# Kernel optimization log

Hardware: AMD Instinct MI355X
Metric: run time of the kernel (lower is better)

The kernel has to match this reference:

```python
import jax, jax.numpy as jnp
import numpy as np

N = 8192      # nodes (= hidden_channels / heads)
E = 262144    # edges (avg degree 32)
IN = 256      # in_channels
H = 8         # heads
C = 32        # out_channels per head
NEG_SLOPE = 0.2


def setup_inputs() -> dict:
    key = jax.random.key(0)
    ks = jax.random.split(key, 8)
    x = jax.random.normal(ks[0], (N, IN), jnp.float32)
    edge_index = jax.random.randint(ks[1], (2, E), 0, N, dtype=jnp.int32)
    lin_w = jax.random.normal(ks[2], (H * C, IN), jnp.float32) * (1.0 / np.sqrt(IN))
    att_src = jax.random.normal(ks[3], (H, C), jnp.float32) * 0.1
    att_dst = jax.random.normal(ks[4], (H, C), jnp.float32) * 0.1
    bias = jax.random.normal(ks[5], (H * C,), jnp.float32) * 0.01
    out_w = jax.random.normal(ks[6], (C, N * H * C), jnp.float32) * (1.0 / np.sqrt(N * H * C))
    out_b = jax.random.normal(ks[7], (C,), jnp.float32) * 0.01
    return {"x": x, "edge_index": edge_index, "lin_w": lin_w, "att_src": att_src,
            "att_dst": att_dst, "bias": bias, "out_w": out_w, "out_b": out_b}


def reference(x, edge_index, lin_w, att_src, att_dst, bias, out_w, out_b):
    n = x.shape[0]
    # PyG GATConv default: add self loops
    loop = jnp.arange(n, dtype=edge_index.dtype)
    src = jnp.concatenate([edge_index[0], loop])  # message sources j
    dst = jnp.concatenate([edge_index[1], loop])  # message targets i
    # per-head linear projection: [n, H, C]
    xh = (x @ lin_w.T).reshape(n, H, C)
    a_src = jnp.einsum('nhc,hc->nh', xh, att_src)  # [n, H]
    a_dst = jnp.einsum('nhc,hc->nh', xh, att_dst)  # [n, H]
    # edge attention logits + segment softmax over incoming edges of each dst
    e = jax.nn.leaky_relu(a_src[src] + a_dst[dst], negative_slope=NEG_SLOPE)  # [E', H]
    m = jax.ops.segment_max(e, dst, num_segments=n)        # [n, H]
    ex = jnp.exp(e - m[dst])
    denom = jax.ops.segment_sum(ex, dst, num_segments=n)   # [n, H]
    alpha = ex / denom[dst]                                 # [E', H]
    # weighted scatter-add aggregation
    agg = jax.ops.segment_sum(alpha[:, :, None] * xh[src], dst, num_segments=n)  # [n, H, C]
    out = agg.reshape(n, H * C) + bias
    # flatten all nodes, dense output layer, softmax
    y = out.reshape(-1) @ out_w.T + out_b  # [C]
    return jax.nn.softmax(y)
```

## Files before the change

### kernel.cpp

```cpp
#include <hip/hip_runtime.h>


namespace {
constexpr int  kN    = 8192;
constexpr int  kE    = 262144;
constexpr int  kTotE = kE + kN;
constexpr long kK    = 2097152;
constexpr int  kNBF  = 2048;
}

typedef float vfloat4 __attribute__((ext_vector_type(4)));

static __device__ __forceinline__ ushort f2bf(float f) {
  unsigned u = __float_as_uint(f);
  return (ushort)((u + 0x7FFFu + ((u >> 16) & 1u)) >> 16);
}
static __device__ __forceinline__ float bf2f(ushort b) {
  return __uint_as_float(((unsigned)b) << 16);
}

__global__ __launch_bounds__(256) void gemm_xh(const float* __restrict__ x,
                                               const float* __restrict__ lw,
                                               float* __restrict__ xh,
                                               ushort* __restrict__ xh_bf) {
  __shared__ float As[16][68];
  __shared__ float Bs[16][68];
  const int t  = threadIdx.x;
  const int tx = t & 15, ty = t >> 4;
  const int rowBase = blockIdx.x * 64;
  const int colBase = blockIdx.y * 64;
  const int lr = t >> 2;
  const int lk = (t & 3) * 4;

  float acc[4][4] = {};
  for (int kc = 0; kc < 256; kc += 16) {
    float4 av = *(const float4*)(x  + (long)(rowBase + lr) * 256 + kc + lk);
    float4 bv = *(const float4*)(lw + (long)(colBase + lr) * 256 + kc + lk);
    __syncthreads();
    As[lk + 0][lr] = av.x; As[lk + 1][lr] = av.y; As[lk + 2][lr] = av.z; As[lk + 3][lr] = av.w;
    Bs[lk + 0][lr] = bv.x; Bs[lk + 1][lr] = bv.y; Bs[lk + 2][lr] = bv.z; Bs[lk + 3][lr] = bv.w;
    __syncthreads();
#pragma unroll
    for (int k = 0; k < 16; k++) {
      float4 a4 = *(const float4*)(&As[k][ty * 4]);
      float4 b4 = *(const float4*)(&Bs[k][tx * 4]);
      float aa[4] = {a4.x, a4.y, a4.z, a4.w};
      float bb[4] = {b4.x, b4.y, b4.z, b4.w};
#pragma unroll
      for (int i = 0; i < 4; i++)
#pragma unroll
        for (int j = 0; j < 4; j++) acc[i][j] += aa[i] * bb[j];
    }
  }
#pragma unroll
  for (int i = 0; i < 4; i++) {
    const long row = rowBase + ty * 4 + i;
    float4 o = make_float4(acc[i][0], acc[i][1], acc[i][2], acc[i][3]);
    *(float4*)(xh + row * 256 + colBase + tx * 4) = o;
    ushort4 ob = make_ushort4(f2bf(o.x), f2bf(o.y), f2bf(o.z), f2bf(o.w));
    *(ushort4*)(xh_bf + row * 256 + colBase + tx * 4) = ob;
  }
}

__global__ __launch_bounds__(256) void att_deg(const float* __restrict__ xh,
                                               const float* __restrict__ att_s,
                                               const float* __restrict__ att_d,
                                               const int* __restrict__ ei,
                                               float* __restrict__ a_src,
                                               float* __restrict__ a_dst,
                                               int* __restrict__ cnt) {
  const int n = blockIdx.x, t = threadIdx.x;
  float v = xh[(long)n * 256 + t];
  float s = v * att_s[t];
  float d = v * att_d[t];
#pragma unroll
  for (int off = 16; off; off >>= 1) {
    s += __shfl_down(s, off, 32);
    d += __shfl_down(d, off, 32);
  }
  if ((t & 31) == 0) {
    a_src[n * 8 + (t >> 5)] = s;
    a_dst[n * 8 + (t >> 5)] = d;
  }
  const int gid = n * 256 + t;
  if (gid < kE) atomicAdd(&cnt[ei[kE + gid]], 1);
}

__global__ __launch_bounds__(1024) void scan_cnt(const int* __restrict__ cnt,
                                                 int* __restrict__ rowptr,
                                                 int* __restrict__ wpos) {
  __shared__ int s[1024];
  const int t = threadIdx.x;
  int v[8]; int sum = 0;
#pragma unroll
  for (int q = 0; q < 8; q++) { v[q] = cnt[t * 8 + q] + 1; sum += v[q]; }
  s[t] = sum;
  __syncthreads();
  for (int off = 1; off < 1024; off <<= 1) {
    int add = (t >= off) ? s[t - off] : 0;
    __syncthreads();
    s[t] += add;
    __syncthreads();
  }
  int excl = s[t] - sum;
#pragma unroll
  for (int q = 0; q < 8; q++) {
    rowptr[t * 8 + q] = excl;
    wpos[t * 8 + q]   = excl;
    excl += v[q];
  }
  if (t == 1023) rowptr[kN] = s[1023];
}

__global__ __launch_bounds__(256) void scatter_csr(const int* __restrict__ ei,
                                                   const float* __restrict__ a_src,
                                                   const float* __restrict__ a_dst,
                                                   int* __restrict__ wpos,
                                                   int* __restrict__ csr,
                                                   float* __restrict__ w8) {
  int idx = blockIdx.x * 256 + threadIdx.x;
  if (idx >= kTotE) return;
  int s, d;
  if (idx < kE) { s = ei[idx]; d = ei[kE + idx]; }
  else          { s = idx - kE; d = s; }
  int pos = atomicAdd(&wpos[d], 1);
  csr[pos] = s;
  float4 s0 = *(const float4*)(a_src + s * 8);
  float4 s1 = *(const float4*)(a_src + s * 8 + 4);
  float4 d0 = *(const float4*)(a_dst + d * 8);
  float4 d1 = *(const float4*)(a_dst + d * 8 + 4);
  float e[8] = {s0.x + d0.x, s0.y + d0.y, s0.z + d0.z, s0.w + d0.w,
                s1.x + d1.x, s1.y + d1.y, s1.z + d1.z, s1.w + d1.w};
  float w[8];
#pragma unroll
  for (int h = 0; h < 8; h++) {
    float ee = (e[h] > 0.f) ? e[h] : 0.2f * e[h];
    w[h] = __expf(ee);
  }
  float4* wp = (float4*)(w8 + (long)pos * 8);
  wp[0] = make_float4(w[0], w[1], w[2], w[3]);
  wp[1] = make_float4(w[4], w[5], w[6], w[7]);
}

__global__ __launch_bounds__(256) void agg_kernel(const ushort* __restrict__ xb,
                                                  const float* __restrict__ w8,
                                                  const int* __restrict__ rowptr,
                                                  const int* __restrict__ csr,
                                                  const float* __restrict__ bias,
                                                  float* __restrict__ out_flat) {
  const int i = blockIdx.x, t = threadIdx.x, h = t >> 5;
  const int beg = rowptr[i], end = rowptr[i + 1];
  float acc = 0.f, den = 0.f;
  int j = beg;
  for (; j + 8 <= end; j += 8) {
    int   s[8]; float w[8]; float f[8];
#pragma unroll
    for (int q = 0; q < 8; q++) s[q] = csr[j + q];
#pragma unroll
    for (int q = 0; q < 8; q++) w[q] = w8[(long)(j + q) * 8 + h];
#pragma unroll
    for (int q = 0; q < 8; q++) f[q] = bf2f(xb[(long)s[q] * 256 + t]);
#pragma unroll
    for (int q = 0; q < 8; q++) { den += w[q]; acc += w[q] * f[q]; }
  }
  for (; j < end; j++) {
    int s0 = csr[j];
    float w0 = w8[(long)j * 8 + h];
    den += w0;
    acc += w0 * bf2f(xb[(long)s0 * 256 + t]);
  }
  out_flat[(long)i * 256 + t] = acc / den + bias[t];
}

__global__ __launch_bounds__(256) void final_dot(const float* __restrict__ of,
                                                 const float* __restrict__ w,
                                                 float* __restrict__ part) {
  const int t = threadIdx.x, b = blockIdx.x;
  const long k = (long)b * 1024 + t * 4;
  float4 f = *(const float4*)(of + k);
  float acc[32];
#pragma unroll
  for (int c = 0; c < 32; c++) {
    vfloat4 wv = __builtin_nontemporal_load((const vfloat4*)(w + (long)c * kK + k));
    acc[c] = wv.x * f.x + wv.y * f.y + wv.z * f.z + wv.w * f.w;
  }
#pragma unroll
  for (int c = 0; c < 32; c++) {
    float v = acc[c];
    v += __shfl_down(v, 32, 64);
    v += __shfl_down(v, 16, 64);
    v += __shfl_down(v, 8, 64);
    v += __shfl_down(v, 4, 64);
    v += __shfl_down(v, 2, 64);
    v += __shfl_down(v, 1, 64);
    acc[c] = v;
  }
  __shared__ float s[4][32];
  const int lane = t & 63, wid = t >> 6;
  if (lane == 0) {
#pragma unroll
    for (int c = 0; c < 32; c++) s[wid][c] = acc[c];
  }
  __syncthreads();
  if (t < 32) part[b * 32 + t] = s[0][t] + s[1][t] + s[2][t] + s[3][t];
}

__global__ __launch_bounds__(1024) void finalize(const float* __restrict__ part,
                                                 const float* __restrict__ ob,
                                                 float* __restrict__ out) {
  __shared__ float s[32][33];
  const int t = threadIdx.x;
  const int c = t & 31, r = t >> 5;
  float sum = 0.f;
  for (int i = r; i < kNBF; i += 32) sum += part[i * 32 + c];
  s[c][r] = sum;
  __syncthreads();
  if (t < 32) {
    float y = ob[t];
#pragma unroll
    for (int r2 = 0; r2 < 32; r2++) y += s[t][r2];
    float m = y;
#pragma unroll
    for (int off = 16; off; off >>= 1) m = fmaxf(m, __shfl_xor(m, off, 32));
    float e = __expf(y - m);
    float d = e;
#pragma unroll
    for (int off = 16; off; off >>= 1) d += __shfl_xor(d, off, 32);
    out[t] = e / d;
  }
}

extern "C" void kernel_launch(void* const* d_in, const int* in_sizes, int n_in,
                              void* d_out, int out_size, void* d_ws, size_t ws_size,
                              hipStream_t stream) {
  (void)in_sizes; (void)n_in; (void)out_size; (void)ws_size;
  const float* x     = (const float*)d_in[0];
  const int*   ei    = (const int*)  d_in[1];
  const float* lin_w = (const float*)d_in[2];
  const float* att_s = (const float*)d_in[3];
  const float* att_d = (const float*)d_in[4];
  const float* bias  = (const float*)d_in[5];
  const float* out_w = (const float*)d_in[6];
  const float* out_b = (const float*)d_in[7];
  float* out = (float*)d_out;

  float*  xh       = (float*)d_ws;
  float*  out_flat = xh + kK;
  float*  a_src    = out_flat + kK;
  float*  a_dst    = a_src + kN * 8;
  float*  part     = a_dst + kN * 8;
  float*  w8       = part + (long)kNBF * 32;
  ushort* xh_bf    = (ushort*)(w8 + (long)kTotE * 8);
  int*    cnt      = (int*)(xh_bf + kK);
  int*    rowptr   = cnt + kN;
  int*    wpos     = rowptr + (kN + 1);
  int*    csr      = wpos + kN;

  (void)hipMemsetAsync(cnt, 0, kN * sizeof(int), stream);
  gemm_xh    <<<dim3(128, 4), 256, 0, stream>>>(x, lin_w, xh, xh_bf);
  att_deg    <<<kN, 256, 0, stream>>>(xh, att_s, att_d, ei, a_src, a_dst, cnt);
  scan_cnt   <<<1, 1024, 0, stream>>>(cnt, rowptr, wpos);
  scatter_csr<<<(kTotE + 255) / 256, 256, 0, stream>>>(ei, a_src, a_dst, wpos, csr, w8);
  agg_kernel <<<kN, 256, 0, stream>>>(xh_bf, w8, rowptr, csr, bias, out_flat);
  final_dot  <<<kNBF, 256, 0, stream>>>(out_flat, out_w, part);
  finalize   <<<1, 1024, 0, stream>>>(part, out_b, out);
}
```

Baseline: 458.2 us.

## Fuse attention logits and degree count into GEMM, and final dot into aggregation

The attention-score projection and in-degree counting move into the GEMM epilogue and prologue. Per-head partial dots are reduced with shuffles and accumulated via float atomics into zeroed a_src/a_dst. The dense output-layer dot is computed per node inside the aggregation kernel, reading out_w directly and writing per-node partials. This removes the fp32 xh and out_flat round trips and two launches. The cost is more float atomics, with nondeterministic summation order, and a finalize that now reduces 8192 partial rows instead of 2048.

Result: slower. 488.1 us (+6.5%).

```diff
diff --git a/kernel.cpp b/kernel.cpp
--- a/kernel.cpp
+++ b/kernel.cpp
@@ -6,7 +6,6 @@
 constexpr int  kE    = 262144;
 constexpr int  kTotE = kE + kN;
 constexpr long kK    = 2097152;
-constexpr int  kNBF  = 2048;
 }
 
 typedef float vfloat4 __attribute__((ext_vector_type(4)));
@@ -19,10 +18,15 @@
   return __uint_as_float(((unsigned)b) << 16);
 }
 
-__global__ __launch_bounds__(256) void gemm_xh(const float* __restrict__ x,
-                                               const float* __restrict__ lw,
-                                               float* __restrict__ xh,
-                                               ushort* __restrict__ xh_bf) {
+__global__ __launch_bounds__(256) void gemm_att_deg(const float* __restrict__ x,
+                                                    const float* __restrict__ lw,
+                                                    const float* __restrict__ att_s,
+                                                    const float* __restrict__ att_d,
+                                                    const int* __restrict__ ei,
+                                                    ushort* __restrict__ xh_bf,
+                                                    float* __restrict__ a_src,
+                                                    float* __restrict__ a_dst,
+                                                    int* __restrict__ cnt) {
   __shared__ float As[16][68];
   __shared__ float Bs[16][68];
   const int t  = threadIdx.x;
@@ -32,6 +36,12 @@
   const int lr = t >> 2;
   const int lk = (t & 3) * 4;
 
+  {
+    const int gid = (blockIdx.y * 128 + blockIdx.x) * 256 + t;
+    atomicAdd(&cnt[ei[kE + gid]], 1);
+    atomicAdd(&cnt[ei[kE + gid + 131072]], 1);
+  }
+
   float acc[4][4] = {};
   for (int kc = 0; kc < 256; kc += 16) {
     float4 av = *(const float4*)(x  + (long)(rowBase + lr) * 256 + kc + lk);
@@ -52,38 +62,34 @@
         for (int j = 0; j < 4; j++) acc[i][j] += aa[i] * bb[j];
     }
   }
+
 #pragma unroll
   for (int i = 0; i < 4; i++) {
     const long row = rowBase + ty * 4 + i;
-    float4 o = make_float4(acc[i][0], acc[i][1], acc[i][2], acc[i][3]);
-    *(float4*)(xh + row * 256 + colBase + tx * 4) = o;
-    ushort4 ob = make_ushort4(f2bf(o.x), f2bf(o.y), f2bf(o.z), f2bf(o.w));
+    ushort4 ob = make_ushort4(f2bf(acc[i][0]), f2bf(acc[i][1]),
+                              f2bf(acc[i][2]), f2bf(acc[i][3]));
     *(ushort4*)(xh_bf + row * 256 + colBase + tx * 4) = ob;
   }
-}
-
-__global__ __launch_bounds__(256) void att_deg(const float* __restrict__ xh,
-                                               const float* __restrict__ att_s,
-                                               const float* __restrict__ att_d,
-                                               const int* __restrict__ ei,
-                                               float* __restrict__ a_src,
-                                               float* __restrict__ a_dst,
-                                               int* __restrict__ cnt) {
-  const int n = blockIdx.x, t = threadIdx.x;
-  float v = xh[(long)n * 256 + t];
-  float s = v * att_s[t];
-  float d = v * att_d[t];
-#pragma unroll
-  for (int off = 16; off; off >>= 1) {
-    s += __shfl_down(s, off, 32);
-    d += __shfl_down(d, off, 32);
-  }
-  if ((t & 31) == 0) {
-    a_src[n * 8 + (t >> 5)] = s;
-    a_dst[n * 8 + (t >> 5)] = d;
-  }
-  const int gid = n * 256 + t;
-  if (gid < kE) atomicAdd(&cnt[ei[kE + gid]], 1);
+
+  const int c0 = colBase + tx * 4;
+  const int h  = (c0 >> 5) & 7;
+  float as_c[4], ad_c[4];
+#pragma unroll
+  for (int j = 0; j < 4; j++) { as_c[j] = att_s[c0 + j]; ad_c[j] = att_d[c0 + j]; }
+#pragma unroll
+  for (int i = 0; i < 4; i++) {
+    float ps = acc[i][0] * as_c[0] + acc[i][1] * as_c[1] +
+               acc[i][2] * as_c[2] + acc[i][3] * as_c[3];
+    float pd = acc[i][0] * ad_c[0] + acc[i][1] * ad_c[1] +
+               acc[i][2] * ad_c[2] + acc[i][3] * ad_c[3];
+    ps += __shfl_down(ps, 1, 64); ps += __shfl_down(ps, 2, 64); ps += __shfl_down(ps, 4, 64);
+    pd += __shfl_down(pd, 1, 64); pd += __shfl_down(pd, 2, 64); pd += __shfl_down(pd, 4, 64);
+    if ((tx & 7) == 0) {
+      const int row = rowBase + ty * 4 + i;
+      atomicAdd(&a_src[row * 8 + h], ps);
+      atomicAdd(&a_dst[row * 8 + h], pd);
+    }
+  }
 }
 
 __global__ __launch_bounds__(1024) void scan_cnt(const int* __restrict__ cnt,
@@ -142,26 +148,27 @@
   wp[1] = make_float4(w[4], w[5], w[6], w[7]);
 }
 
-__global__ __launch_bounds__(256) void agg_kernel(const ushort* __restrict__ xb,
-                                                  const float* __restrict__ w8,
-                                                  const int* __restrict__ rowptr,
-                                                  const int* __restrict__ csr,
-                                                  const float* __restrict__ bias,
-                                                  float* __restrict__ out_flat) {
+__global__ __launch_bounds__(256) void agg_dot(const ushort* __restrict__ xb,
+                                               const float* __restrict__ w8,
+                                               const int* __restrict__ rowptr,
+                                               const int* __restrict__ csr,
+                                               const float* __restrict__ bias,
+                                               const float* __restrict__ w,
+                                               float* __restrict__ part) {
   const int i = blockIdx.x, t = threadIdx.x, h = t >> 5;
   const int beg = rowptr[i], end = rowptr[i + 1];
   float acc = 0.f, den = 0.f;
   int j = beg;
   for (; j + 8 <= end; j += 8) {
-    int   s[8]; float w[8]; float f[8];
+    int s[8]; float ww[8]; float f[8];
 #pragma unroll
     for (int q = 0; q < 8; q++) s[q] = csr[j + q];
 #pragma unroll
-    for (int q = 0; q < 8; q++) w[q] = w8[(long)(j + q) * 8 + h];
+    for (int q = 0; q < 8; q++) ww[q] = w8[(long)(j + q) * 8 + h];
 #pragma unroll
     for (int q = 0; q < 8; q++) f[q] = bf2f(xb[(long)s[q] * 256 + t]);
 #pragma unroll
-    for (int q = 0; q < 8; q++) { den += w[q]; acc += w[q] * f[q]; }
+    for (int q = 0; q < 8; q++) { den += ww[q]; acc += ww[q] * f[q]; }
   }
   for (; j < end; j++) {
     int s0 = csr[j];
@@ -169,40 +176,31 @@
     den += w0;
     acc += w0 * bf2f(xb[(long)s0 * 256 + t]);
   }
-  out_flat[(long)i * 256 + t] = acc / den + bias[t];
-}
-
-__global__ __launch_bounds__(256) void final_dot(const float* __restrict__ of,
-                                                 const float* __restrict__ w,
-                                                 float* __restrict__ part) {
-  const int t = threadIdx.x, b = blockIdx.x;
-  const long k = (long)b * 1024 + t * 4;
-  float4 f = *(const float4*)(of + k);
-  float acc[32];
-#pragma unroll
-  for (int c = 0; c < 32; c++) {
-    vfloat4 wv = __builtin_nontemporal_load((const vfloat4*)(w + (long)c * kK + k));
-    acc[c] = wv.x * f.x + wv.y * f.y + wv.z * f.z + wv.w * f.w;
-  }
-#pragma unroll
-  for (int c = 0; c < 32; c++) {
-    float v = acc[c];
+  __shared__ float s_of[256];
+  s_of[t] = acc / den + bias[t];
+  __syncthreads();
+
+  const int q = t & 63, w4 = t >> 6;
+  float4 fv = *(const float4*)(s_of + q * 4);
+  float pr[8];
+#pragma unroll
+  for (int m = 0; m < 8; m++) {
+    const int c = w4 + m * 4;
+    vfloat4 wv = __builtin_nontemporal_load(
+        (const vfloat4*)(w + (long)c * kK + (long)i * 256 + q * 4));
+    pr[m] = wv.x * fv.x + wv.y * fv.y + wv.z * fv.z + wv.w * fv.w;
+  }
+#pragma unroll
+  for (int m = 0; m < 8; m++) {
+    float v = pr[m];
     v += __shfl_down(v, 32, 64);
     v += __shfl_down(v, 16, 64);
     v += __shfl_down(v, 8, 64);
     v += __shfl_down(v, 4, 64);
     v += __shfl_down(v, 2, 64);
     v += __shfl_down(v, 1, 64);
-    acc[c] = v;
-  }
-  __shared__ float s[4][32];
-  const int lane = t & 63, wid = t >> 6;
-  if (lane == 0) {
-#pragma unroll
-    for (int c = 0; c < 32; c++) s[wid][c] = acc[c];
-  }
-  __syncthreads();
-  if (t < 32) part[b * 32 + t] = s[0][t] + s[1][t] + s[2][t] + s[3][t];
+    if (q == 0) part[(long)i * 32 + w4 + m * 4] = v;
+  }
 }
 
 __global__ __launch_bounds__(1024) void finalize(const float* __restrict__ part,
@@ -212,7 +210,7 @@
   const int t = threadIdx.x;
   const int c = t & 31, r = t >> 5;
   float sum = 0.f;
-  for (int i = r; i < kNBF; i += 32) sum += part[i * 32 + c];
+  for (int i = r; i < kN; i += 32) sum += part[(long)i * 32 + c];
   s[c][r] = sum;
   __syncthreads();
   if (t < 32) {
@@ -244,24 +242,21 @@
   const float* out_b = (const float*)d_in[7];
   float* out = (float*)d_out;
 
-  float*  xh       = (float*)d_ws;
-  float*  out_flat = xh + kK;
-  float*  a_src    = out_flat + kK;
-  float*  a_dst    = a_src + kN * 8;
-  float*  part     = a_dst + kN * 8;
-  float*  w8       = part + (long)kNBF * 32;
-  ushort* xh_bf    = (ushort*)(w8 + (long)kTotE * 8);
-  int*    cnt      = (int*)(xh_bf + kK);
-  int*    rowptr   = cnt + kN;
-  int*    wpos     = rowptr + (kN + 1);
-  int*    csr      = wpos + kN;
-
-  (void)hipMemsetAsync(cnt, 0, kN * sizeof(int), stream);
-  gemm_xh    <<<dim3(128, 4), 256, 0, stream>>>(x, lin_w, xh, xh_bf);
-  att_deg    <<<kN, 256, 0, stream>>>(xh, att_s, att_d, ei, a_src, a_dst, cnt);
-  scan_cnt   <<<1, 1024, 0, stream>>>(cnt, rowptr, wpos);
-  scatter_csr<<<(kTotE + 255) / 256, 256, 0, stream>>>(ei, a_src, a_dst, wpos, csr, w8);
-  agg_kernel <<<kN, 256, 0, stream>>>(xh_bf, w8, rowptr, csr, bias, out_flat);
-  final_dot  <<<kNBF, 256, 0, stream>>>(out_flat, out_w, part);
-  finalize   <<<1, 1024, 0, stream>>>(part, out_b, out);
-}
+  int*    cnt    = (int*)d_ws;
+  float*  a_src  = (float*)(cnt + kN);
+  float*  a_dst  = a_src + kN * 8;
+  ushort* xh_bf  = (ushort*)(a_dst + kN * 8);
+  float*  w8     = (float*)(xh_bf + kK);
+  float*  part   = w8 + (long)kTotE * 8;
+  int*    rowptr = (int*)(part + (long)kN * 32);
+  int*    wpos   = rowptr + (kN + 1);
+  int*    csr    = wpos + kN;
+
+  (void)hipMemsetAsync(cnt, 0, (kN + 2 * kN * 8) * sizeof(int), stream);
+  gemm_att_deg<<<dim3(128, 4), 256, 0, stream>>>(x, lin_w, att_s, att_d, ei,
+                                                 xh_bf, a_src, a_dst, cnt);
+  scan_cnt    <<<1, 1024, 0, stream>>>(cnt, rowptr, wpos);
+  scatter_csr <<<kTotE / 256, 256, 0, stream>>>(ei, a_src, a_dst, wpos, csr, w8);
+  agg_dot     <<<kN, 256, 0, stream>>>(xh_bf, w8, rowptr, csr, bias, out_w, part);
+  finalize    <<<1, 1024, 0, stream>>>(part, out_b, out);
+}
```
